# Kernel tuning notes

Measured on AMD Instinct MI355X. Metric: run time of the kernel, lower is better.

The kernel has to match this reference:

```python
import jax, jax.numpy as jnp
import numpy as np

EPS = 1e-8
H, DH = 4, 8
HID = H * DH  # 32
FF = 20       # 4 * dim
C = 5         # channels per degree


def snorm(x):
    # grad-safe L2 norm over last axis
    return jnp.sqrt(jnp.sum(x * x, axis=-1) + 1e-12)


def _ln(v, gamma, beta):
    mu = v.mean(-1, keepdims=True)
    sd = v.std(-1, keepdims=True) + EPS
    return (v - mu) / sd * gamma + beta


def norm_se3(x0, x1, g, b):
    # equivariant norm: transform per-channel invariant norms, keep orientation (phase)
    n0 = jnp.abs(x0)
    y0 = jnp.sign(x0) * jax.nn.gelu(_ln(n0, g[0], b[0]))
    n1 = snorm(x1)                                        # (b,n,c)
    y1 = x1 / n1[..., None] * jax.nn.gelu(_ln(n1, g[1], b[1]))[..., None]
    return y0, y1


def attention(x0, x1, coors, adjm, Wq, Mk, Mv, R1, rb1, R2, rb2, Wo0, Wo1):
    b, n, c = x0.shape
    rel = coors[:, None, :, :] - coors[:, :, None, :]     # (b,i,j,3): x_j - x_i
    dist = jnp.sqrt(jnp.sum(rel * rel, -1, keepdims=True) + 1e-12)
    u = rel / dist                                        # unit directions
    # radial net -> per-edge kernel coefficients for each degree-pair/basis (k and v)
    phi = jax.nn.relu(dist @ R1 + rb1) @ R2 + rb2         # (b,i,j,12*HID)
    (k00, k10, k01, kI, kU, kX, v00, v10, v01, vI, vU, vX) = jnp.split(phi, 12, -1)

    def edge_feats(M, p00, p10, p01, pI, pU, pX):
        y00 = jnp.einsum('bjc,ch->bjh', x0, M[0])
        y10 = jnp.einsum('bjcm,ch->bjhm', x1, M[1])
        y01 = jnp.einsum('bjc,ch->bjh', x0, M[2])
        yI = jnp.einsum('bjcm,ch->bjhm', x1, M[3])
        yU = jnp.einsum('bjcm,ch->bjhm', x1, M[4])
        yX = jnp.einsum('bjcm,ch->bjhm', x1, M[5])
        # degree-0 messages: (0->0) scalar and (1->0) vector.dot(u) paths
        e0 = p00 * y00[:, None] + p10 * jnp.einsum('bjhm,bijm->bijh', y10, u)
        un = u[:, :, :, None, :]                          # (b,i,j,1,3)
        # degree-1 messages: closed-form equivariant bases u*s, I, u(u.v), u x v
        e1 = (p01[..., None] * y01[:, None, :, :, None] * un
              + pI[..., None] * yI[:, None]
              + pU[..., None] * jnp.einsum('bjhm,bijm->bijh', yU, u)[..., None] * un
              + pX[..., None] * jnp.cross(un, yX[:, None]))
        return e0, e1

    k0, k1 = edge_feats(Mk, k00, k10, k01, kI, kU, kX)
    v0, v1 = edge_feats(Mv, v00, v10, v01, vI, vU, vX)

    q0 = jnp.einsum('bic,ch->bih', x0, Wq[0]).reshape(b, n, H, DH)
    q1 = jnp.einsum('bicm,ch->bihm', x1, Wq[1]).reshape(b, n, H, DH, 3)
    logits = (jnp.einsum('bihd,bijhd->bhij', q0, k0.reshape(b, n, n, H, DH))
              + jnp.einsum('bihdm,bijhdm->bhij', q1, k1.reshape(b, n, n, H, DH, 3)))
    logits = logits / jnp.asarray(DH, x0.dtype) ** 0.5
    logits = jnp.where(adjm[:, None], logits, -1e9)       # sparse-neighbor mask
    attn = jax.nn.softmax(logits, axis=-1)
    o0 = jnp.einsum('bhij,bijhd->bihd', attn, v0.reshape(b, n, n, H, DH)).reshape(b, n, HID)
    o1 = jnp.einsum('bhij,bijhdm->bihdm', attn, v1.reshape(b, n, n, H, DH, 3)).reshape(b, n, HID, 3)
    return o0 @ Wo0, jnp.einsum('bnhm,hc->bncm', o1, Wo1)


def feedforward(x0, x1, Wf1, Wf2, gs, bs):
    h0 = jax.nn.gelu(jnp.einsum('bnc,cf->bnf', x0, Wf1[0]))
    h1 = jnp.einsum('bncm,cf->bnfm', x1, Wf1[1])
    h1 = h1 * jax.nn.sigmoid(snorm(h1) * gs + bs)[..., None]   # norm-gated nonlin (equivariant)
    return jnp.einsum('bnf,fc->bnc', h0, Wf2[0]), jnp.einsum('bnfm,fc->bncm', h1, Wf2[1])


def _forward(feats, coors, adj_mat, Wq, Mk, Mv, R1, rb1, R2, rb2, Wo0, Wo1, gnA, bnA, gnF, bnF, Wf1, Wf2, gs, bs, Wh1, bh1, Wh2, bh2):
    b, n, _ = feats.shape
    a = adj_mat.astype(jnp.float32)
    # num_adj_degrees=2: attend over 1-hop OR 2-hop neighbors (plus self)
    adjm = adj_mat | ((a @ a) > 0) | jnp.eye(n, dtype=bool)
    x0 = feats
    x1 = jnp.zeros(feats.shape + (3,), feats.dtype)       # input fiber has only degree-0
    x0n, x1n = norm_se3(x0, x1, gnA, bnA)
    d0, d1 = attention(x0n, x1n, coors, adjm, Wq, Mk, Mv, R1, rb1, R2, rb2, Wo0, Wo1)
    x0, x1 = x0 + d0, x1 + d1
    x0n, x1n = norm_se3(x0, x1, gnF, bnF)
    f0, f1 = feedforward(x0n, x1n, Wf1, Wf2, gs, bs)
    x0, x1 = x0 + f0, x1 + f1
    pooled = x0.mean(axis=1)                              # mean pool type-0 features
    h = jax.nn.relu(pooled @ Wh1 + bh1)
    out = h @ Wh2 + bh2                                   # (b, 9)
    return out.reshape(-1, 3, 3)


def setup_inputs():
    key = jax.random.key(0)
    ks = jax.random.split(key, 16)
    B, N = 2, 256
    g = lambda i, shape, s: jax.random.normal(ks[i], shape, jnp.float32) * s
    feats = g(0, (B, N, C), 1.0)
    coors = g(1, (B, N, 3), 3.0)
    r = jax.random.uniform(ks[2], (B, N, N))
    adj = r < 0.03
    adj = (adj | jnp.swapaxes(adj, 1, 2)) & ~jnp.eye(N, dtype=bool)
    s5, sh, sf, s128 = C ** -0.5, HID ** -0.5, FF ** -0.5, 128 ** -0.5
    return dict(
        feats=feats, coors=coors, adj_mat=adj,
        Wq=g(3, (2, C, HID), s5), Mk=g(4, (6, C, HID), s5), Mv=g(5, (6, C, HID), s5),
        R1=g(6, (1, 32), 1.0), rb1=jnp.zeros(32), R2=g(7, (32, 12 * HID), 32 ** -0.5), rb2=jnp.zeros(12 * HID),
        Wo0=g(8, (HID, C), sh), Wo1=g(9, (HID, C), sh),
        gnA=jnp.ones((2, C)), bnA=jnp.zeros((2, C)), gnF=jnp.ones((2, C)), bnF=jnp.zeros((2, C)),
        Wf1=g(10, (2, C, FF), s5), Wf2=g(11, (2, FF, C), sf), gs=jnp.ones(FF), bs=jnp.zeros(FF),
        Wh1=g(12, (C, 128), s5), bh1=jnp.zeros(128), Wh2=g(13, (128, 9), s128), bh2=jnp.zeros(9))


def reference(feats, coors, adj_mat, Wq, Mk, Mv, R1, rb1, R2, rb2, Wo0, Wo1, gnA, bnA, gnF, bnF, Wf1, Wf2, gs, bs, Wh1, bh1, Wh2, bh2):
    return _forward(feats, coors, adj_mat, Wq, Mk, Mv, R1, rb1, R2, rb2, Wo0, Wo1, gnA, bnA, gnF, bnF, Wf1, Wf2, gs, bs, Wh1, bh1, Wh2, bh2)
```

## Files before the change

kernel.cpp:

```cpp
#include <hip/hip_runtime.h>
#include <math.h>

#define NN 256
#define CC 5
#define HIDD 32


__device__ __forceinline__ float gelu_tanh(float x) {
    float x3 = x * x * x;
    return 0.5f * x * (1.0f + tanhf(0.7978845608028654f * (x + 0.044715f * x3)));
}
__device__ __forceinline__ float sgnf(float x) {
    return (x > 0.f) ? 1.f : ((x < 0.f) ? -1.f : 0.f);
}

#define TROW 9
#define TSZ (33 * TROW)

__global__ __launch_bounds__(256) void fused_all(
    const float* __restrict__ coors,
    const int* __restrict__ adj,
    const float* __restrict__ feats,
    const float* __restrict__ Wq0, const float* __restrict__ Mk0, const float* __restrict__ Mv0,
    const float* __restrict__ gnA0, const float* __restrict__ bnA0,
    const float* __restrict__ R1, const float* __restrict__ rb1,
    const float* __restrict__ R2, const float* __restrict__ rb2,
    const float* __restrict__ Wo0,
    const float* __restrict__ gnF0, const float* __restrict__ bnF0,
    const float* __restrict__ Wf10,
    const float* __restrict__ Wf20,
    const float* __restrict__ Wh1, const float* __restrict__ bh1,
    const float* __restrict__ Wh2, const float* __restrict__ bh2,
    float* __restrict__ xfin,
    int* __restrict__ ctr, const int* __restrict__ refw,
    float* __restrict__ out)
{
    int node = blockIdx.x;
    int b = node >> 8, i = node & 255;
    int tid = threadIdx.x;
    int j = tid;
    int lane = tid & 63, wave = tid >> 6;

    __shared__ float4 sT[4 * TSZ];
    __shared__ float2 kv[32][32];
    __shared__ float2 srr[32];
    __shared__ float srb2k[32], srb2v[32];
    __shared__ float tt[32], sts[32];
    __shared__ unsigned int smask[33];
    __shared__ float q0s[32];
    __shared__ float Wo0t[5][32];
    __shared__ int nlist[NN];
    __shared__ int ncnt;
    __shared__ float wredm[4][4], wreds[4][4], hm[4], hs[4];
    __shared__ float ew[4][5], x0as[5], xfs[5], h0s[20];
    __shared__ float part[2][5][25], pooled[10], hdn[2][128];

    int av = adj[(size_t)(b * NN + i) * NN + j];

    for (int idx = tid; idx < 1024; idx += 256) {
        int w = idx >> 5, hd = idx & 31;
        kv[w][hd] = make_float2(R2[w * 384 + hd], R2[w * 384 + 192 + hd]);
    }
    if (tid < 32) {
        srr[tid] = make_float2(R1[tid], rb1[tid]);
        srb2k[tid] = rb2[tid];
        srb2v[tid] = rb2[192 + tid];
    }
    if (tid < 160) Wo0t[tid / 32][tid % 32] = Wo0[(tid % 32) * 5 + tid / 32];
    if (tid == 0) ncnt = 0;

    float dx = coors[(b * NN + j) * 3 + 0] - coors[(b * NN + i) * 3 + 0];
    float dy = coors[(b * NN + j) * 3 + 1] - coors[(b * NN + i) * 3 + 1];
    float dz = coors[(b * NN + j) * 3 + 2] - coors[(b * NN + i) * 3 + 2];
    float dist = sqrtf(dx * dx + dy * dy + dz * dz + 1e-12f);

    float x0n[CC];
    {
        const float* f = feats + (size_t)(b * NN + j) * CC;
        float fv[CC], n0[CC];
        float mu = 0.f;
#pragma unroll
        for (int c = 0; c < CC; c++) { fv[c] = f[c]; n0[c] = fabsf(fv[c]); mu += n0[c]; }
        mu *= (1.0f / CC);
        float var = 0.f;
#pragma unroll
        for (int c = 0; c < CC; c++) { float d = n0[c] - mu; var += d * d; }
        var *= (1.0f / CC);
        float sd = sqrtf(var) + 1e-8f;
#pragma unroll
        for (int c = 0; c < CC; c++) {
            float ln = (n0[c] - mu) / sd * gnA0[c] + bnA0[c];
            x0n[c] = sgnf(fv[c]) * gelu_tanh(ln);
        }
    }
    __syncthreads();

    if (tid < 32) {
        float r = srr[tid].x;
        tt[tid] = (r != 0.f) ? (-srr[tid].y / r) : -3.0e38f;
    }
    if (tid < 32) {
        float t = tt[tid];
        int rank = 0;
        for (int k = 0; k < 32; k++) {
            float tk = tt[k];
            rank += (tk < t) || (tk == t && k < tid);
        }
        sts[rank] = t;
    }
    if (tid < 33) {
        float rep = (tid == 0) ? (sts[0] - 1.0f)
                  : (tid == 32) ? (sts[31] + 1.0f)
                  : 0.5f * (sts[tid - 1] + sts[tid]);
        unsigned int m = 0;
        for (int w = 0; w < 32; w++) {
            float2 rr = srr[w];
            if (fmaf(rr.x, rep, rr.y) > 0.f) m |= (1u << w);
        }
        smask[tid] = m;
    }
    if (tid < 32) {
        const float* f = feats + (size_t)(b * NN + i) * CC;
        float fv[CC], n0[CC], xi[CC];
        float mu = 0.f;
#pragma unroll
        for (int c = 0; c < CC; c++) { fv[c] = f[c]; n0[c] = fabsf(fv[c]); mu += n0[c]; }
        mu *= (1.0f / CC);
        float var = 0.f;
#pragma unroll
        for (int c = 0; c < CC; c++) { float d = n0[c] - mu; var += d * d; }
        var *= (1.0f / CC);
        float sd = sqrtf(var) + 1e-8f;
#pragma unroll
        for (int c = 0; c < CC; c++) {
            float ln = (n0[c] - mu) / sd * gnA0[c] + bnA0[c];
            xi[c] = sgnf(fv[c]) * gelu_tanh(ln);
        }
        float q = 0.f;
#pragma unroll
        for (int c = 0; c < CC; c++) q = fmaf(xi[c], Wq0[c * HIDD + tid], q);
        q0s[tid] = q;
    }
    if (av) { int p = atomicAdd(&ncnt, 1); nlist[p] = j; }

    float ykr[32];
#pragma unroll
    for (int hd = 0; hd < 32; hd++) ykr[hd] = 0.f;
#pragma unroll
    for (int c = 0; c < CC; c++) {
        float xc = x0n[c];
#pragma unroll
        for (int hd = 0; hd < 32; hd++)
            ykr[hd] = fmaf(xc, Mk0[c * HIDD + hd], ykr[hd]);
    }
    __syncthreads();

    int okacc = (av != 0) || (i == j);
    {
        int cnt = ncnt;
        for (int t = 0; t < cnt; t += 8) {
            int idxs[8], vv[8];
#pragma unroll
            for (int k = 0; k < 8; k++) {
                int u = t + k;
                idxs[k] = nlist[(u < cnt) ? u : t];
            }
#pragma unroll
            for (int k = 0; k < 8; k++)
                vv[k] = adj[(size_t)(b * NN + idxs[k]) * NN + j];
#pragma unroll
            for (int k = 0; k < 8; k++) okacc |= vv[k];
        }
    }
    for (int idx = tid; idx < 33 * 32; idx += 256) {
        int p = idx >> 5, hd = idx & 31;
        unsigned int m = smask[p];
        float A = 0.f, Bv = 0.f, Cv = 0.f, Dv = 0.f;
        while (m) {
            int w = __ffs(m) - 1;
            m &= (m - 1);
            float2 rr = srr[w];
            float2 kw = kv[w][hd];
            A  = fmaf(rr.x, kw.x, A);  Bv = fmaf(rr.y, kw.x, Bv);
            Cv = fmaf(rr.x, kw.y, Cv); Dv = fmaf(rr.y, kw.y, Dv);
        }
        Bv += srb2k[hd];
        Dv += srb2v[hd];
        float* tf = (float*)sT;
        tf[(0 * TSZ + p * TROW) * 4 + hd] = A;
        tf[(1 * TSZ + p * TROW) * 4 + hd] = Bv;
        tf[(2 * TSZ + p * TROW) * 4 + hd] = Cv;
        tf[(3 * TSZ + p * TROW) * 4 + hd] = Dv;
    }
    __syncthreads();

    int p = 0;
#pragma unroll
    for (int k = 0; k < 32; k++) p += (sts[k] < dist) ? 1 : 0;

    const float4* Ap = sT + 0 * TSZ + p * TROW;
    const float4* Bp = sT + 1 * TSZ + p * TROW;
    const float4* Cp = sT + 2 * TSZ + p * TROW;
    const float4* Dp = sT + 3 * TSZ + p * TROW;
    const float4* q04 = (const float4*)q0s;

    float lg[4] = {0.f, 0.f, 0.f, 0.f};
#pragma unroll
    for (int q = 0; q < 8; q++) {
        float4 a = Ap[q], bb = Bp[q], qq = q04[q];
        int h = q >> 1;
        lg[h] = fmaf(fmaf(dist, a.x, bb.x) * qq.x, ykr[4 * q + 0], lg[h]);
        lg[h] = fmaf(fmaf(dist, a.y, bb.y) * qq.y, ykr[4 * q + 1], lg[h]);
        lg[h] = fmaf(fmaf(dist, a.z, bb.z) * qq.z, ykr[4 * q + 2], lg[h]);
        lg[h] = fmaf(fmaf(dist, a.w, bb.w) * qq.w, ykr[4 * q + 3], lg[h]);
    }
    {
        const float invs = 0.35355339059327379f;
        bool ok = okacc != 0;
#pragma unroll
        for (int h = 0; h < 4; h++) lg[h] = ok ? lg[h] * invs : -1e9f;
    }

    float attn[4];
#pragma unroll
    for (int h = 0; h < 4; h++) {
        float v = lg[h];
        for (int off = 32; off; off >>= 1) v = fmaxf(v, __shfl_xor(v, off, 64));
        if (lane == 0) wredm[h][wave] = v;
    }
    __syncthreads();
    if (tid < 4) hm[tid] = fmaxf(fmaxf(wredm[tid][0], wredm[tid][1]), fmaxf(wredm[tid][2], wredm[tid][3]));
    __syncthreads();
#pragma unroll
    for (int h = 0; h < 4; h++) lg[h] = expf(lg[h] - hm[h]);
#pragma unroll
    for (int h = 0; h < 4; h++) {
        float v = lg[h];
        for (int off = 32; off; off >>= 1) v += __shfl_xor(v, off, 64);
        if (lane == 0) wreds[h][wave] = v;
    }
    __syncthreads();
    if (tid < 4) hs[tid] = wreds[tid][0] + wreds[tid][1] + wreds[tid][2] + wreds[tid][3];
    __syncthreads();
#pragma unroll
    for (int h = 0; h < 4; h++) attn[h] = lg[h] / hs[h];

    float yvr[32];
#pragma unroll
    for (int hd = 0; hd < 32; hd++) yvr[hd] = 0.f;
#pragma unroll
    for (int c = 0; c < CC; c++) {
        float xc = x0n[c];
#pragma unroll
        for (int hd = 0; hd < 32; hd++)
            yvr[hd] = fmaf(xc, Mv0[c * HIDD + hd], yvr[hd]);
    }

    float e[5] = {0.f, 0.f, 0.f, 0.f, 0.f};
#pragma unroll
    for (int q = 0; q < 8; q++) {
        float4 c4 = Cp[q], d4 = Dp[q];
        float at = attn[q >> 1];
        float4 pv;
        pv.x = at * fmaf(dist, c4.x, d4.x) * yvr[4 * q + 0];
        pv.y = at * fmaf(dist, c4.y, d4.y) * yvr[4 * q + 1];
        pv.z = at * fmaf(dist, c4.z, d4.z) * yvr[4 * q + 2];
        pv.w = at * fmaf(dist, c4.w, d4.w) * yvr[4 * q + 3];
#pragma unroll
        for (int c = 0; c < 5; c++) {
            float4 w4 = ((const float4*)Wo0t[c])[q];
            e[c] = fmaf(pv.x, w4.x, fmaf(pv.y, w4.y, fmaf(pv.z, w4.z, fmaf(pv.w, w4.w, e[c]))));
        }
    }
    for (int off = 32; off; off >>= 1)
#pragma unroll
        for (int c = 0; c < 5; c++) e[c] += __shfl_xor(e[c], off, 64);
    if (lane == 0)
#pragma unroll
        for (int c = 0; c < 5; c++) ew[wave][c] = e[c];
    __syncthreads();

    if (wave != 0) return;

    if (lane < 5) {
        float d0 = ew[0][lane] + ew[1][lane] + ew[2][lane] + ew[3][lane];
        x0as[lane] = feats[node * 5 + lane] + d0;
    }
    if (lane < 5) {
        float x0a[5], n0[5];
        float mu = 0.f;
#pragma unroll
        for (int c = 0; c < 5; c++) { x0a[c] = x0as[c]; n0[c] = fabsf(x0a[c]); mu += n0[c]; }
        mu *= 0.2f;
        float var = 0.f;
#pragma unroll
        for (int c = 0; c < 5; c++) { float d = n0[c] - mu; var += d * d; }
        var *= 0.2f;
        float sd = sqrtf(var) + 1e-8f;
        float ln = (n0[lane] - mu) / sd * gnF0[lane] + bnF0[lane];
        xfs[lane] = sgnf(x0a[lane]) * gelu_tanh(ln);
    }
    if (lane < 20) {
        float s = 0.f;
#pragma unroll
        for (int c = 0; c < 5; c++) s = fmaf(xfs[c], Wf10[c * 20 + lane], s);
        h0s[lane] = gelu_tanh(s);
    }
    if (lane < 5) {
        float f0 = 0.f;
        for (int f = 0; f < 20; f++) f0 = fmaf(h0s[f], Wf20[f * 5 + lane], f0);
        xfin[node * 5 + lane] = x0as[lane] + f0;
    }

    __threadfence();
    int slast = 0, base = 0;
    if (lane == 0) {
        base = __hip_atomic_load(refw, __ATOMIC_RELAXED, __HIP_MEMORY_SCOPE_AGENT);
        int old = __hip_atomic_fetch_add(ctr, 1, __ATOMIC_ACQ_REL, __HIP_MEMORY_SCOPE_AGENT);
        slast = ((old - base) == 511) ? 1 : 0;
    }
    slast = __shfl(slast, 0, 64);
    if (!slast) return;

    __threadfence();

    for (int tpl = lane; tpl < 250; tpl += 64) {
        int bb = tpl / 125, r = tpl % 125, c = r / 25, grp = r % 25;
        float s = 0.f;
        for (int ii = grp; ii < NN; ii += 25) s += xfin[(bb * NN + ii) * 5 + c];
        part[bb][c][grp] = s;
    }
    if (lane < 10) {
        int bb = lane / 5, c = lane % 5;
        float s = 0.f;
        for (int g = 0; g < 25; g++) s += part[bb][c][g];
        pooled[lane] = s * (1.0f / NN);
    }
    for (int kk = lane; kk < 256; kk += 64) {
        int bb = kk >> 7, k = kk & 127;
        float s = bh1[k];
#pragma unroll
        for (int c = 0; c < 5; c++) s = fmaf(pooled[bb * 5 + c], Wh1[c * 128 + k], s);
        hdn[bb][k] = fmaxf(s, 0.f);
    }
    if (lane < 18) {
        int bb = lane / 9, o = lane % 9;
        float s = bh2[o];
        for (int k = 0; k < 128; k++) s = fmaf(hdn[bb][k], Wh2[k * 9 + o], s);
        out[bb * 9 + o] = s;
    }
    if (lane == 0) {
        __hip_atomic_store(ctr, base, __ATOMIC_RELAXED, __HIP_MEMORY_SCOPE_AGENT);
    }
}

extern "C" void kernel_launch(void* const* d_in, const int* in_sizes, int n_in,
                              void* d_out, int out_size, void* d_ws, size_t ws_size,
                              hipStream_t stream) {
    const float* feats = (const float*)d_in[0];
    const float* coors = (const float*)d_in[1];
    const int*   adj   = (const int*)d_in[2];
    const float* Wq    = (const float*)d_in[3];
    const float* Mk    = (const float*)d_in[4];
    const float* Mv    = (const float*)d_in[5];
    const float* R1    = (const float*)d_in[6];
    const float* rb1   = (const float*)d_in[7];
    const float* R2    = (const float*)d_in[8];
    const float* rb2   = (const float*)d_in[9];
    const float* Wo0   = (const float*)d_in[10];
    const float* gnA   = (const float*)d_in[12];
    const float* bnA   = (const float*)d_in[13];
    const float* gnF   = (const float*)d_in[14];
    const float* bnF   = (const float*)d_in[15];
    const float* Wf1   = (const float*)d_in[16];
    const float* Wf2   = (const float*)d_in[17];
    const float* Wh1   = (const float*)d_in[20];
    const float* bh1   = (const float*)d_in[21];
    const float* Wh2   = (const float*)d_in[22];
    const float* bh2   = (const float*)d_in[23];
    float* out = (float*)d_out;

    float* xfin = (float*)d_ws;
    int* ctr    = (int*)((char*)d_ws + 16384);
    const int* refw = (const int*)((char*)d_ws + 16400);

    hipLaunchKernelGGL(fused_all, dim3(512), dim3(256), 0, stream,
                       coors, adj, feats, Wq, Mk, Mv, gnA, bnA, R1, rb1, R2, rb2,
                       Wo0, gnF, bnF, Wf1, Wf2, Wh1, bh1, Wh2, bh2,
                       xfin, ctr, refw, out);
}
```

Baseline: 155.4 us.

## Split last-block head reduction into a separate kernel and drop softmax barriers

The atomic-counter last-block pattern that ran the pooled MLP head inside the fused kernel is replaced by a second single-block kernel launched after the attention kernel. This removes the threadfence and atomic from every block. Separately, the softmax max and sum reductions are now computed redundantly by every thread from shared partials, which drops two __syncthreads per block. The cost is an extra kernel launch plus its dependency gap.

Result: faster. 125.3 us (-19.3%).

```diff
diff --git a/kernel.cpp b/kernel.cpp
--- a/kernel.cpp
+++ b/kernel.cpp
@@ -17,7 +17,7 @@
 #define TROW 9
 #define TSZ (33 * TROW)
 
-__global__ __launch_bounds__(256) void fused_all(
+__global__ __launch_bounds__(256) void fused_attn(
     const float* __restrict__ coors,
     const int* __restrict__ adj,
     const float* __restrict__ feats,
@@ -29,11 +29,7 @@
     const float* __restrict__ gnF0, const float* __restrict__ bnF0,
     const float* __restrict__ Wf10,
     const float* __restrict__ Wf20,
-    const float* __restrict__ Wh1, const float* __restrict__ bh1,
-    const float* __restrict__ Wh2, const float* __restrict__ bh2,
-    float* __restrict__ xfin,
-    int* __restrict__ ctr, const int* __restrict__ refw,
-    float* __restrict__ out)
+    float* __restrict__ xfin)
 {
     int node = blockIdx.x;
     int b = node >> 8, i = node & 255;
@@ -51,9 +47,8 @@
     __shared__ float Wo0t[5][32];
     __shared__ int nlist[NN];
     __shared__ int ncnt;
-    __shared__ float wredm[4][4], wreds[4][4], hm[4], hs[4];
+    __shared__ float wredm[4][4], wreds[4][4];
     __shared__ float ew[4][5], x0as[5], xfs[5], h0s[20];
-    __shared__ float part[2][5][25], pooled[10], hdn[2][128];
 
     int av = adj[(size_t)(b * NN + i) * NN + j];
 
@@ -229,10 +224,12 @@
         if (lane == 0) wredm[h][wave] = v;
     }
     __syncthreads();
-    if (tid < 4) hm[tid] = fmaxf(fmaxf(wredm[tid][0], wredm[tid][1]), fmaxf(wredm[tid][2], wredm[tid][3]));
-    __syncthreads();
-#pragma unroll
-    for (int h = 0; h < 4; h++) lg[h] = expf(lg[h] - hm[h]);
+    float hmv[4];
+#pragma unroll
+    for (int h = 0; h < 4; h++)
+        hmv[h] = fmaxf(fmaxf(wredm[h][0], wredm[h][1]), fmaxf(wredm[h][2], wredm[h][3]));
+#pragma unroll
+    for (int h = 0; h < 4; h++) lg[h] = expf(lg[h] - hmv[h]);
 #pragma unroll
     for (int h = 0; h < 4; h++) {
         float v = lg[h];
@@ -240,10 +237,11 @@
         if (lane == 0) wreds[h][wave] = v;
     }
     __syncthreads();
-    if (tid < 4) hs[tid] = wreds[tid][0] + wreds[tid][1] + wreds[tid][2] + wreds[tid][3];
-    __syncthreads();
-#pragma unroll
-    for (int h = 0; h < 4; h++) attn[h] = lg[h] / hs[h];
+#pragma unroll
+    for (int h = 0; h < 4; h++) {
+        float hsv = wreds[h][0] + wreds[h][1] + wreds[h][2] + wreds[h][3];
+        attn[h] = lg[h] / hsv;
+    }
 
     float yvr[32];
 #pragma unroll
@@ -311,46 +309,43 @@
         for (int f = 0; f < 20; f++) f0 = fmaf(h0s[f], Wf20[f * 5 + lane], f0);
         xfin[node * 5 + lane] = x0as[lane] + f0;
     }
-
-    __threadfence();
-    int slast = 0, base = 0;
-    if (lane == 0) {
-        base = __hip_atomic_load(refw, __ATOMIC_RELAXED, __HIP_MEMORY_SCOPE_AGENT);
-        int old = __hip_atomic_fetch_add(ctr, 1, __ATOMIC_ACQ_REL, __HIP_MEMORY_SCOPE_AGENT);
-        slast = ((old - base) == 511) ? 1 : 0;
-    }
-    slast = __shfl(slast, 0, 64);
-    if (!slast) return;
-
-    __threadfence();
-
-    for (int tpl = lane; tpl < 250; tpl += 64) {
-        int bb = tpl / 125, r = tpl % 125, c = r / 25, grp = r % 25;
+}
+
+__global__ __launch_bounds__(256) void head_mlp(const float* __restrict__ xfin,
+                         const float* __restrict__ Wh1, const float* __restrict__ bh1,
+                         const float* __restrict__ Wh2, const float* __restrict__ bh2,
+                         float* __restrict__ out) {
+    __shared__ float part[2][5][25];
+    __shared__ float pooled[10];
+    __shared__ float hdn[2][128];
+    int tid = threadIdx.x;
+    if (tid < 250) {
+        int b = tid / 125, r = tid % 125, c = r / 25, grp = r % 25;
         float s = 0.f;
-        for (int ii = grp; ii < NN; ii += 25) s += xfin[(bb * NN + ii) * 5 + c];
-        part[bb][c][grp] = s;
-    }
-    if (lane < 10) {
-        int bb = lane / 5, c = lane % 5;
+        for (int i = grp; i < NN; i += 25) s += xfin[(b * NN + i) * 5 + c];
+        part[b][c][grp] = s;
+    }
+    __syncthreads();
+    if (tid < 10) {
+        int b = tid / 5, c = tid % 5;
         float s = 0.f;
-        for (int g = 0; g < 25; g++) s += part[bb][c][g];
-        pooled[lane] = s * (1.0f / NN);
-    }
-    for (int kk = lane; kk < 256; kk += 64) {
-        int bb = kk >> 7, k = kk & 127;
+        for (int g = 0; g < 25; g++) s += part[b][c][g];
+        pooled[tid] = s * (1.0f / NN);
+    }
+    __syncthreads();
+    {
+        int b = tid >> 7, k = tid & 127;
         float s = bh1[k];
 #pragma unroll
-        for (int c = 0; c < 5; c++) s = fmaf(pooled[bb * 5 + c], Wh1[c * 128 + k], s);
-        hdn[bb][k] = fmaxf(s, 0.f);
-    }
-    if (lane < 18) {
-        int bb = lane / 9, o = lane % 9;
+        for (int c = 0; c < 5; c++) s = fmaf(pooled[b * 5 + c], Wh1[c * 128 + k], s);
+        hdn[b][k] = fmaxf(s, 0.f);
+    }
+    __syncthreads();
+    if (tid < 18) {
+        int b = tid / 9, o = tid % 9;
         float s = bh2[o];
-        for (int k = 0; k < 128; k++) s = fmaf(hdn[bb][k], Wh2[k * 9 + o], s);
-        out[bb * 9 + o] = s;
-    }
-    if (lane == 0) {
-        __hip_atomic_store(ctr, base, __ATOMIC_RELAXED, __HIP_MEMORY_SCOPE_AGENT);
+        for (int k = 0; k < 128; k++) s = fmaf(hdn[b][k], Wh2[k * 9 + o], s);
+        out[b * 9 + o] = s;
     }
 }
 
@@ -381,11 +376,10 @@
     float* out = (float*)d_out;
 
     float* xfin = (float*)d_ws;
-    int* ctr    = (int*)((char*)d_ws + 16384);
-    const int* refw = (const int*)((char*)d_ws + 16400);
-
-    hipLaunchKernelGGL(fused_all, dim3(512), dim3(256), 0, stream,
+
+    hipLaunchKernelGGL(fused_attn, dim3(512), dim3(256), 0, stream,
                        coors, adj, feats, Wq, Mk, Mv, gnA, bnA, R1, rb1, R2, rb2,
-                       Wo0, gnF, bnF, Wf1, Wf2, Wh1, bh1, Wh2, bh2,
-                       xfin, ctr, refw, out);
-}
+                       Wo0, gnF, bnF, Wf1, Wf2, xfin);
+    hipLaunchKernelGGL(head_mlp, dim3(1), dim3(256), 0, stream,
+                       xfin, Wh1, bh1, Wh2, bh2, out);
+}
```
